# Optimization experiments

Measured on AMD Instinct MI355X. Metric: run time of the kernel, lower is better.

The kernel has to match this reference:

```python
import jax, jax.numpy as jnp
import numpy as np

B, M, H = 1024, 32, 2
D = 64
N_ENT = 500000
N_REL = 32


def setup_inputs() -> dict:
    key = jax.random.key(0)
    k1, k2, k3, k4 = jax.random.split(key, 4)
    edge_index = jax.random.randint(k1, (B, 2), 0, N_ENT, dtype=jnp.int64)
    # column 0: head entity ids, column 1: relation ids; keep both < N_REL so both are in-range
    ripple_sets = jax.random.randint(k2, (H, B, M, 2), 0, N_REL, dtype=jnp.int64)
    entity_emb = jax.random.normal(k3, (N_ENT, D), dtype=jnp.float32)
    relation_emb = jax.random.normal(k4, (N_REL, D * D), dtype=jnp.float32)
    # padding_idx=0 -> row 0 is zeros
    entity_emb = entity_emb.at[0].set(0.0)
    relation_emb = relation_emb.at[0].set(0.0)
    return {
        "edge_index": edge_index,
        "ripple_sets": ripple_sets,
        "entity_emb": entity_emb,
        "relation_emb": relation_emb,
    }


def reference(edge_index, ripple_sets, entity_emb, relation_emb):
    d = entity_emb.shape[1]
    item = entity_emb[edge_index[:, 1]]            # [B, d]
    u = jnp.zeros_like(item)                       # [B, d]
    for hop in range(ripple_sets.shape[0]):        # small fixed hop count
        rs = ripple_sets[hop]                      # [B, M, 2]
        R = relation_emb[rs[:, :, 1]].reshape(rs.shape[0], -1, d, d)  # [B, M, d, d]
        h = entity_emb[rs[:, :, 0]]                # [B, M, d]
        Rh = jnp.einsum('bmij,bmj->bmi', R, h)     # [B, M, d]
        vRh = jnp.einsum('bmi,bi->bm', Rh, item)   # [B, M]
        p = jax.nn.softmax(vRh, axis=1)            # [B, M]
        u = u + jnp.einsum('bm,bmd->bd', p, h)     # weighted sum of tails (t == h)
    return jnp.sum(u * item, axis=1, keepdims=True)  # [B, 1]
```

## Files before the change

kernel.cpp:

```cpp
#include <hip/hip_runtime.h>
#include <math.h>

#define BB   1024
#define MM   32
#define HH   2
#define DD   64
#define NREL 32
#define TPB  256

#define HS 65
#define QS 65

__global__ __launch_bounds__(TPB) void ripple_fused(
    const int* __restrict__ edge_index,
    const int* __restrict__ ripple_sets,
    const float* __restrict__ entity_emb,
    const float* __restrict__ relation_emb,
    float* __restrict__ out)
{
    __shared__ float item_s[DD];
    __shared__ float h_s[HH * MM * HS];
    __shared__ float q_s[NREL * QS];
    __shared__ int   head_s[HH * MM];
    __shared__ int   rel_s[HH * MM];
    __shared__ float v_s[HH * MM];
    __shared__ float p_s[HH * MM];

    const int b   = blockIdx.x;
    const int tid = threadIdx.x;

    if (tid < DD) {
        int item_idx = edge_index[2 * b + 1];
        item_s[tid] = entity_emb[(size_t)item_idx * DD + tid];
    }
    if (tid < HH * MM) {
        int hop = tid >> 5, m = tid & 31;
        size_t base = ((size_t)(hop * BB + b) * MM + m) * 2;
        head_s[tid] = ripple_sets[base];
        rel_s[tid]  = ripple_sets[base + 1];
    }
    __syncthreads();

    for (int k = 0; k < 4; ++k) {
        int idx = tid + TPB * k;
        int row = idx >> 4;
        int c4  = idx & 15;
        const float4 v = *(const float4*)(entity_emb + (size_t)head_s[row] * DD + c4 * 4);
        float* dst = h_s + row * HS + c4 * 4;
        dst[0] = v.x; dst[1] = v.y; dst[2] = v.z; dst[3] = v.w;
    }

    for (int k = 0; k < 2; ++k) {
        int task = tid + TPB * k;
        int r  = task >> 4;
        int c4 = task & 15;
        const float* Rp = relation_emb + (size_t)r * DD * DD + c4 * 4;
        float4 acc = {0.f, 0.f, 0.f, 0.f};
        #pragma unroll
        for (int i = 0; i < DD; ++i) {
            float it = item_s[i];
            const float4 rv = *(const float4*)(Rp + i * DD);
            acc.x += it * rv.x; acc.y += it * rv.y;
            acc.z += it * rv.z; acc.w += it * rv.w;
        }
        float* dst = q_s + r * QS + c4 * 4;
        dst[0] = acc.x; dst[1] = acc.y; dst[2] = acc.z; dst[3] = acc.w;
    }
    __syncthreads();

    if (tid < HH * MM) {
        int r = rel_s[tid];
        const float* qp = q_s + r * QS;
        const float* hp = h_s + tid * HS;
        float acc = 0.f;
        #pragma unroll
        for (int j = 0; j < DD; ++j) acc += qp[j] * hp[j];
        v_s[tid] = acc;
    }
    __syncthreads();

    if (tid < HH) {
        const float* vv = v_s + tid * MM;
        float* pp = p_s + tid * MM;
        float mx = vv[0];
        for (int m = 1; m < MM; ++m) mx = fmaxf(mx, vv[m]);
        float s = 0.f;
        for (int m = 0; m < MM; ++m) { float e = expf(vv[m] - mx); pp[m] = e; s += e; }
        float inv = 1.f / s;
        for (int m = 0; m < MM; ++m) pp[m] *= inv;
    }
    __syncthreads();

    if (tid < DD) {
        float u = 0.f;
        #pragma unroll
        for (int t = 0; t < HH * MM; ++t) u += p_s[t] * h_s[t * HS + tid];
        float prod = u * item_s[tid];
        #pragma unroll
        for (int off = 32; off > 0; off >>= 1) prod += __shfl_down(prod, off, 64);
        if (tid == 0) out[b] = prod;
    }
}

extern "C" void kernel_launch(void* const* d_in, const int* in_sizes, int n_in,
                              void* d_out, int out_size, void* d_ws, size_t ws_size,
                              hipStream_t stream) {
    const int*   edge_index   = (const int*)d_in[0];
    const int*   ripple_sets  = (const int*)d_in[1];
    const float* entity_emb   = (const float*)d_in[2];
    const float* relation_emb = (const float*)d_in[3];
    float* out = (float*)d_out;
    (void)in_sizes; (void)n_in; (void)out_size; (void)d_ws; (void)ws_size;

    ripple_fused<<<dim3(BB), dim3(TPB), 0, stream>>>(
        edge_index, ripple_sets, entity_emb, relation_emb, out);
}
```

Baseline: 186.2 us.

## Split q=item·R into a separate tiled kernel sharing R across batch rows

Moves the per-batch item-times-relation-matrix product into its own kernel, where each block stages one 64x64 relation matrix in shared memory and reuses it for 32 batch rows. In the old kernel every block streamed all 32 relation matrices from global memory. The results are written to a workspace buffer of size B x NREL x 64, and the apply kernel gathers the q row for each (hop, m). This costs an extra kernel launch and a round trip of about 8 MB through global memory, and it assumes the workspace is large enough.

```diff
diff --git a/kernel.cpp b/kernel.cpp
--- a/kernel.cpp
+++ b/kernel.cpp
@@ -6,21 +6,69 @@
 #define HH   2
 #define DD   64
 #define NREL 32
-#define TPB  256
+#define TBB  32
+
+__global__ __launch_bounds__(256) void compute_q(
+    const int* __restrict__ edge_index,
+    const float* __restrict__ entity_emb,
+    const float* __restrict__ relation_emb,
+    float* __restrict__ qout)
+{
+    __shared__ float R_s[DD * DD];
+    __shared__ float item_s[TBB * 68];
+
+    const int r   = blockIdx.y;
+    const int b0  = blockIdx.x * TBB;
+    const int tid = threadIdx.x;
+
+    const float4* Rg = (const float4*)(relation_emb + (size_t)r * DD * DD);
+    #pragma unroll
+    for (int k = 0; k < 4; ++k)
+        ((float4*)R_s)[tid + 256 * k] = Rg[tid + 256 * k];
+
+    #pragma unroll
+    for (int k = 0; k < 2; ++k) {
+        int idx = tid + 256 * k;
+        int bl  = idx >> 4;
+        int c4  = idx & 15;
+        int ei  = edge_index[2 * (b0 + bl) + 1];
+        ((float4*)(item_s + bl * 68))[c4] =
+            *(const float4*)(entity_emb + (size_t)ei * DD + c4 * 4);
+    }
+    __syncthreads();
+
+    const int j4  = (tid & 15) * 4;
+    const int bl0 = tid >> 4;
+    float4 acc0 = {0.f, 0.f, 0.f, 0.f};
+    float4 acc1 = {0.f, 0.f, 0.f, 0.f};
+    #pragma unroll 8
+    for (int i = 0; i < DD; ++i) {
+        const float4 rv = *(const float4*)(R_s + i * DD + j4);
+        const float a0 = item_s[bl0 * 68 + i];
+        const float a1 = item_s[(bl0 + 16) * 68 + i];
+        acc0.x += a0 * rv.x; acc0.y += a0 * rv.y;
+        acc0.z += a0 * rv.z; acc0.w += a0 * rv.w;
+        acc1.x += a1 * rv.x; acc1.y += a1 * rv.y;
+        acc1.z += a1 * rv.z; acc1.w += a1 * rv.w;
+    }
+    size_t q0 = ((size_t)(b0 + bl0) * NREL + r) * DD + j4;
+    size_t q1 = ((size_t)(b0 + bl0 + 16) * NREL + r) * DD + j4;
+    *(float4*)(qout + q0) = acc0;
+    *(float4*)(qout + q1) = acc1;
+}
 
 #define HS 65
-#define QS 65
 
-__global__ __launch_bounds__(TPB) void ripple_fused(
+__global__ __launch_bounds__(256) void ripple_apply(
     const int* __restrict__ edge_index,
     const int* __restrict__ ripple_sets,
     const float* __restrict__ entity_emb,
-    const float* __restrict__ relation_emb,
+    const float* __restrict__ qg,
     float* __restrict__ out)
 {
     __shared__ float item_s[DD];
     __shared__ float h_s[HH * MM * HS];
-    __shared__ float q_s[NREL * QS];
+    __shared__ float q_s[HH * MM * HS];
     __shared__ int   head_s[HH * MM];
     __shared__ int   rel_s[HH * MM];
     __shared__ float v_s[HH * MM];
@@ -41,36 +89,22 @@
     }
     __syncthreads();
 
+    #pragma unroll
     for (int k = 0; k < 4; ++k) {
-        int idx = tid + TPB * k;
+        int idx = tid + 256 * k;
         int row = idx >> 4;
         int c4  = idx & 15;
-        const float4 v = *(const float4*)(entity_emb + (size_t)head_s[row] * DD + c4 * 4);
-        float* dst = h_s + row * HS + c4 * 4;
-        dst[0] = v.x; dst[1] = v.y; dst[2] = v.z; dst[3] = v.w;
-    }
-
-    for (int k = 0; k < 2; ++k) {
-        int task = tid + TPB * k;
-        int r  = task >> 4;
-        int c4 = task & 15;
-        const float* Rp = relation_emb + (size_t)r * DD * DD + c4 * 4;
-        float4 acc = {0.f, 0.f, 0.f, 0.f};
-        #pragma unroll
-        for (int i = 0; i < DD; ++i) {
-            float it = item_s[i];
-            const float4 rv = *(const float4*)(Rp + i * DD);
-            acc.x += it * rv.x; acc.y += it * rv.y;
-            acc.z += it * rv.z; acc.w += it * rv.w;
-        }
-        float* dst = q_s + r * QS + c4 * 4;
-        dst[0] = acc.x; dst[1] = acc.y; dst[2] = acc.z; dst[3] = acc.w;
+        const float4 hv = *(const float4*)(entity_emb + (size_t)head_s[row] * DD + c4 * 4);
+        float* hd = h_s + row * HS + c4 * 4;
+        hd[0] = hv.x; hd[1] = hv.y; hd[2] = hv.z; hd[3] = hv.w;
+        const float4 qv = *(const float4*)(qg + ((size_t)b * NREL + rel_s[row]) * DD + c4 * 4);
+        float* qd = q_s + row * HS + c4 * 4;
+        qd[0] = qv.x; qd[1] = qv.y; qd[2] = qv.z; qd[3] = qv.w;
     }
     __syncthreads();
 
     if (tid < HH * MM) {
-        int r = rel_s[tid];
-        const float* qp = q_s + r * QS;
+        const float* qp = q_s + tid * HS;
         const float* hp = h_s + tid * HS;
         float acc = 0.f;
         #pragma unroll
@@ -110,8 +144,11 @@
     const float* entity_emb   = (const float*)d_in[2];
     const float* relation_emb = (const float*)d_in[3];
     float* out = (float*)d_out;
-    (void)in_sizes; (void)n_in; (void)out_size; (void)d_ws; (void)ws_size;
+    float* qbuf = (float*)d_ws;
+    (void)in_sizes; (void)n_in; (void)out_size; (void)ws_size;
 
-    ripple_fused<<<dim3(BB), dim3(TPB), 0, stream>>>(
-        edge_index, ripple_sets, entity_emb, relation_emb, out);
+    compute_q<<<dim3(BB / TBB, NREL), dim3(256), 0, stream>>>(
+        edge_index, entity_emb, relation_emb, qbuf);
+    ripple_apply<<<dim3(BB), dim3(256), 0, stream>>>(
+        edge_index, ripple_sets, entity_emb, qbuf, out);
 }
```

New measurement: 175.2 us. 5.9% less time.
